# Optimization experiments

Hardware: AMD Instinct MI355X
Metric: run time of the kernel (lower is better)

The kernel has to match this reference:

```python
import jax, jax.numpy as jnp
import numpy as np

DIM = 128
HEADS = 4
WS = 7
SHIFT = 3
MLP_HIDDEN = 512
B, H, W = 8, 112, 112


def _rel_pos_index(ws):
    coords = np.stack(np.meshgrid(np.arange(ws), np.arange(ws), indexing='ij'))  # 2,ws,ws
    flat = coords.reshape(2, -1)  # 2, ws*ws
    rel = (flat[:, :, None] - flat[:, None, :]).transpose(1, 2, 0)  # N,N,2
    rel[:, :, 0] += ws - 1
    rel[:, :, 1] += ws - 1
    rel[:, :, 0] *= 2 * ws - 1
    return rel.sum(-1).astype(np.int32)  # N,N


def setup_inputs() -> dict:
    key = jax.random.key(0)
    ks = jax.random.split(key, 12)
    s = 0.02
    return {
        'x': jax.random.normal(ks[0], (B, DIM, H, W), jnp.float32),
        'norm1_g': jnp.ones((DIM,), jnp.float32),
        'norm1_b': jnp.zeros((DIM,), jnp.float32),
        'qkv_w': jax.random.normal(ks[1], (DIM, 3 * DIM), jnp.float32) * s,
        'qkv_b': jnp.zeros((3 * DIM,), jnp.float32),
        'rel_bias_table': jax.random.normal(ks[2], ((2 * WS - 1) ** 2, HEADS), jnp.float32) * s,
        'rel_index': jnp.asarray(_rel_pos_index(WS)),
        'proj_w': jax.random.normal(ks[3], (DIM, DIM), jnp.float32) * s,
        'proj_b': jnp.zeros((DIM,), jnp.float32),
        'norm2_g': jnp.ones((DIM,), jnp.float32),
        'norm2_b': jnp.zeros((DIM,), jnp.float32),
        'fc1_w': jax.random.normal(ks[4], (DIM, MLP_HIDDEN), jnp.float32) * s,
        'fc1_b': jnp.zeros((MLP_HIDDEN,), jnp.float32),
        'fc2_w': jax.random.normal(ks[5], (MLP_HIDDEN, DIM), jnp.float32) * s,
        'fc2_b': jnp.zeros((DIM,), jnp.float32),
    }


def _ln(x, g, b, eps=1e-5):
    m = jnp.mean(x, axis=-1, keepdims=True)
    v = jnp.var(x, axis=-1, keepdims=True)
    return (x - m) * jax.lax.rsqrt(v + eps) * g + b


def _swin_fwd(x, norm1_g, norm1_b, qkv_w, qkv_b, rel_bias_table, rel_index,
              proj_w, proj_b, norm2_g, norm2_b, fc1_w, fc1_b, fc2_w, fc2_b):
    Bb, C, Hh, Ww = x.shape
    x = x.reshape(Bb, C, Hh * Ww).transpose(0, 2, 1)  # B, L, C
    shortcut = x
    x = _ln(x, norm1_g, norm1_b)
    x = x.reshape(Bb, Hh, Ww, C)
    # H, W are multiples of WS here, so no padding needed (pad_r = pad_b = 0)
    if SHIFT > 0:
        x = jnp.roll(x, (-SHIFT, -SHIFT), axis=(1, 2))
    nH, nW = Hh // WS, Ww // WS
    # window partition -> (num_windows, N, C)
    xw = x.reshape(Bb, nH, WS, nW, WS, C).transpose(0, 1, 3, 2, 4, 5).reshape(-1, WS * WS, C)
    NWIN, N = xw.shape[0], WS * WS
    hd = C // HEADS
    qkv = (xw @ qkv_w + qkv_b).reshape(NWIN, N, 3, HEADS, hd).transpose(2, 0, 3, 1, 4)
    q, k, v = qkv[0], qkv[1], qkv[2]  # each (NWIN, HEADS, N, hd)
    scale = hd ** -0.5
    attn = jnp.einsum('whnd,whmd->whnm', q * scale, k)
    bias = rel_bias_table[rel_index.reshape(-1)].reshape(N, N, HEADS).transpose(2, 0, 1)
    attn = jax.nn.softmax(attn + bias[None], axis=-1)
    out = jnp.einsum('whnm,whmd->whnd', attn, v)  # NWIN, HEADS, N, hd
    out = out.transpose(0, 2, 1, 3).reshape(NWIN, N, C) @ proj_w + proj_b
    # window reverse
    x = out.reshape(Bb, nH, nW, WS, WS, C).transpose(0, 1, 3, 2, 4, 5).reshape(Bb, Hh, Ww, C)
    if SHIFT > 0:
        x = jnp.roll(x, (SHIFT, SHIFT), axis=(1, 2))
    x = x.reshape(Bb, Hh * Ww, C)
    x = shortcut + x
    h = _ln(x, norm2_g, norm2_b)
    h = jax.nn.gelu(h @ fc1_w + fc1_b, approximate=False) @ fc2_w + fc2_b
    x = x + h
    return x.transpose(0, 2, 1).reshape(Bb, C, Hh, Ww)


def reference(x, norm1_g, norm1_b, qkv_w, qkv_b, rel_bias_table, rel_index,
              proj_w, proj_b, norm2_g, norm2_b, fc1_w, fc1_b, fc2_w, fc2_b):
    return _swin_fwd(x, norm1_g, norm1_b, qkv_w, qkv_b, rel_bias_table, rel_index,
                     proj_w, proj_b, norm2_g, norm2_b, fc1_w, fc1_b, fc2_w, fc2_b)
```

## Files before the change

### kernel.cpp

```cpp
#include <hip/hip_runtime.h>
#include <hip/hip_bf16.h>
#include <math.h>

typedef __bf16 bf16;
typedef __bf16 bf16x8 __attribute__((ext_vector_type(8)));
typedef float f32x4 __attribute__((ext_vector_type(4)));

#define MFMA(a,b,c) __builtin_amdgcn_mfma_f32_16x16x32_bf16(a,b,c,0,0,0)

static __device__ __forceinline__ int swz256(int row, int kb){ return row*256 + (kb ^ ((row&7)<<4)); }
static __device__ __forceinline__ int swz128(int row, int kb){ return row*128 + (kb ^ ((row&7)<<4)); }
static __device__ __forceinline__ int swz64 (int row, int kb){ return row*64  + (kb ^ ((row&3)<<4)); }

__global__ void k_pack(const float* __restrict__ W, bf16* __restrict__ outp, int K, int N) {
    int idx = blockIdx.x*256 + threadIdx.x;
    int total = (N >> 4) * (K >> 5) * 64;
    if (idx >= total) return;
    int l = idx & 63, f = idx >> 6;
    int KF = K >> 5;
    int kf = f % KF, nf = f / KF;
    int n = nf*16 + (l & 15), k0 = kf*32 + (l >> 4)*8;
    bf16x8 v;
    for (int j = 0; j < 8; ++j) v[j] = (bf16)W[(size_t)(k0+j)*N + n];
    *(bf16x8*)(outp + (size_t)idx*8) = v;
}

__global__ void k_bias(const float* __restrict__ table, const int* __restrict__ ridx,
                       float* __restrict__ bias49) {
    int idx = blockIdx.x*256 + threadIdx.x;
    if (idx >= 2401) return;
    int ri = ridx[idx];
    for (int h = 0; h < 4; ++h) bias49[h*2401 + idx] = table[ri*4 + h];
}

__global__ void k_zero(uint4* __restrict__ xw4) {
    int idx = blockIdx.x*256 + threadIdx.x;
    if (idx >= 2048*240) return;
    int win = idx / 240, rem = idx - win*240;
    xw4[(size_t)win*1024 + 784 + rem] = make_uint4(0,0,0,0);
}

__global__ void __launch_bounds__(256) k_ln1(const float* __restrict__ x,
                                             const float* __restrict__ g1,
                                             const float* __restrict__ b1,
                                             bf16* __restrict__ xw) {
    __shared__ float T[128*113];
    __shared__ float meanL[112], rstdL[112];
    __shared__ float gL[128], bL[128];
    int tid = threadIdx.x;
    int b = blockIdx.x / 112, h = blockIdx.x - (blockIdx.x/112)*112;
    if (tid < 128) { gL[tid] = g1[tid]; bL[tid] = b1[tid]; }
    const float* xp = x + (size_t)b*128*12544 + h*112;
    for (int e = tid; e < 14336; e += 256) {
        int c = e / 112, w = e - c*112;
        T[c*113 + w] = xp[(size_t)c*12544 + w];
    }
    __syncthreads();
    if (tid < 224) {
        int w = tid >> 1, q = tid & 1;
        float s = 0.f, s2 = 0.f;
        for (int i = 0; i < 64; ++i) { float v = T[(q*64 + i)*113 + w]; s += v; s2 += v*v; }
        s  += __shfl_xor(s, 1, 64);
        s2 += __shfl_xor(s2, 1, 64);
        if (q == 0) {
            float m = s * 0.0078125f;
            float var = s2 * 0.0078125f - m*m;
            meanL[w] = m; rstdL[w] = rsqrtf(var + 1e-5f);
        }
    }
    __syncthreads();
    int hr = h + 109; if (hr >= 112) hr -= 112;
    int wh = hr / 7, nr = hr - wh*7;
    for (int e = tid; e < 14336; e += 256) {
        int w = e >> 7, c = e & 127;
        int wr = w + 109; if (wr >= 112) wr -= 112;
        int wwi = wr / 7, nc = wr - wwi*7;
        int win = b*256 + wh*16 + wwi;
        int n = nr*7 + nc;
        float v = (T[c*113 + w] - meanL[w]) * rstdL[w] * gL[c] + bL[c];
        xw[((size_t)win*64 + n)*128 + c] = (bf16)v;
    }
}

__global__ void __launch_bounds__(256, 4) k_attn(const bf16* __restrict__ xw,
                                              const bf16x8* __restrict__ wqkv,
                                              const float* __restrict__ qkv_b,
                                              const bf16x8* __restrict__ wproj,
                                              const float* __restrict__ proj_b,
                                              const float* __restrict__ bias49,
                                              bf16* __restrict__ x1p) {
    __shared__ char lds[49152];
    const int tid = threadIdx.x;
    const int l = tid & 63, wv = tid >> 6;
    const int win = blockIdx.x;
    const int lrow = l & 15, lk = l >> 4;
    char* X  = lds;
    char* VT = lds + wv*4096;
    char* Q  = lds + 16384 + wv*8192;
    char* Kt = Q + 4096;
    char* P  = Q;
    char* O  = lds + 16384;

    {
        const uint4* src = (const uint4*)(xw + (size_t)win*8192);
        for (int it = 0; it < 4; ++it) {
            int unit = it*256 + tid;
            int row = unit >> 4, s = unit & 15;
            *(uint4*)(X + swz256(row, s*16)) = src[unit];
        }
    }
    __syncthreads();

    {
        f32x4 qa[4][2], ka[4][2];
        float qb0 = qkv_b[      wv*32 + lrow], qb1 = qkv_b[      wv*32 + 16 + lrow];
        float kb0 = qkv_b[128 + wv*32 + lrow], kb1 = qkv_b[128 + wv*32 + 16 + lrow];
        for (int mf = 0; mf < 4; ++mf) for (int r = 0; r < 4; ++r) {
            qa[mf][0][r] = qb0; qa[mf][1][r] = qb1;
            ka[mf][0][r] = kb0; ka[mf][1][r] = kb1;
        }
        for (int kk = 0; kk < 4; ++kk) {
            bf16x8 a[4];
            for (int mf = 0; mf < 4; ++mf)
                a[mf] = *(const bf16x8*)(X + swz256(mf*16 + lrow, kk*64 + lk*16));
            for (int nf2 = 0; nf2 < 2; ++nf2) {
                bf16x8 bq = wqkv[(( (    wv*2 + nf2)*4 + kk)*64) + l];
                bf16x8 bk = wqkv[(( (8 + wv*2 + nf2)*4 + kk)*64) + l];
                for (int mf = 0; mf < 4; ++mf) {
                    qa[mf][nf2] = MFMA(a[mf], bq, qa[mf][nf2]);
                    ka[mf][nf2] = MFMA(a[mf], bk, ka[mf][nf2]);
                }
            }
        }
        const float scale = 0.17677669529663687f;
        for (int mf = 0; mf < 4; ++mf) for (int nf2 = 0; nf2 < 2; ++nf2)
            for (int r = 0; r < 4; ++r) {
                int row = mf*16 + lk*4 + r;
                int col = nf2*16 + lrow;
                *(bf16*)(Q  + swz64(row, col*2)) = (bf16)(qa[mf][nf2][r] * scale);
                *(bf16*)(Kt + swz64(row, col*2)) = (bf16)(ka[mf][nf2][r]);
            }
    }
    f32x4 va[4][2];
    {
        float vb0 = qkv_b[256 + wv*32 + lrow], vb1 = qkv_b[256 + wv*32 + 16 + lrow];
        for (int mf = 0; mf < 4; ++mf) for (int r = 0; r < 4; ++r) {
            va[mf][0][r] = vb0; va[mf][1][r] = vb1;
        }
        for (int kk = 0; kk < 4; ++kk) {
            bf16x8 a[4];
            for (int mf = 0; mf < 4; ++mf)
                a[mf] = *(const bf16x8*)(X + swz256(mf*16 + lrow, kk*64 + lk*16));
            for (int nf2 = 0; nf2 < 2; ++nf2) {
                bf16x8 bv = wqkv[(((16 + wv*2 + nf2)*4 + kk)*64) + l];
                for (int mf = 0; mf < 4; ++mf)
                    va[mf][nf2] = MFMA(a[mf], bv, va[mf][nf2]);
            }
        }
    }
    __syncthreads();
    for (int mf = 0; mf < 4; ++mf) for (int nf2 = 0; nf2 < 2; ++nf2)
        for (int r = 0; r < 4; ++r) {
            int row = mf*16 + lk*4 + r;
            int col = nf2*16 + lrow;
            *(bf16*)(VT + swz128(col, row*2)) = (bf16)(va[mf][nf2][r]);
        }

    f32x4 s[4][4];
    {
        const float* bh = bias49 + wv*2401;
        for (int mf = 0; mf < 4; ++mf) for (int nf = 0; nf < 4; ++nf)
            for (int r = 0; r < 4; ++r) {
                int row = mf*16 + lk*4 + r, col = nf*16 + lrow;
                float bv;
                if (col >= 49) bv = -1e30f;
                else if (row < 49) bv = bh[row*49 + col];
                else bv = 0.f;
                s[mf][nf][r] = bv;
            }
        bf16x8 aq[4], bk4[4];
        for (int mf = 0; mf < 4; ++mf) aq[mf]  = *(const bf16x8*)(Q  + swz64(mf*16 + lrow, lk*16));
        for (int nf = 0; nf < 4; ++nf) bk4[nf] = *(const bf16x8*)(Kt + swz64(nf*16 + lrow, lk*16));
        for (int mf = 0; mf < 4; ++mf) for (int nf = 0; nf < 4; ++nf)
            s[mf][nf] = MFMA(aq[mf], bk4[nf], s[mf][nf]);
    }
    for (int mf = 0; mf < 4; ++mf) for (int r = 0; r < 4; ++r) {
        float mx = -3e38f;
        for (int nf = 0; nf < 4; ++nf) mx = fmaxf(mx, s[mf][nf][r]);
        for (int d = 1; d < 16; d <<= 1) mx = fmaxf(mx, __shfl_xor(mx, d, 64));
        float sum = 0.f;
        for (int nf = 0; nf < 4; ++nf) { float p = __expf(s[mf][nf][r] - mx); s[mf][nf][r] = p; sum += p; }
        for (int d = 1; d < 16; d <<= 1) sum += __shfl_xor(sum, d, 64);
        float inv = 1.0f / sum;
        for (int nf = 0; nf < 4; ++nf) s[mf][nf][r] *= inv;
    }
    for (int mf = 0; mf < 4; ++mf) for (int nf = 0; nf < 4; ++nf)
        for (int r = 0; r < 4; ++r) {
            int row = mf*16 + lk*4 + r, col = nf*16 + lrow;
            *(bf16*)(P + swz128(row, col*2)) = (bf16)(s[mf][nf][r]);
        }

    f32x4 o[4][2];
    for (int mf = 0; mf < 4; ++mf) for (int nf = 0; nf < 2; ++nf)
        for (int r = 0; r < 4; ++r) o[mf][nf][r] = 0.f;
    for (int kf = 0; kf < 2; ++kf) {
        bf16x8 ap[4], bv2[2];
        for (int mf = 0; mf < 4; ++mf)
            ap[mf] = *(const bf16x8*)(P + swz128(mf*16 + lrow, kf*64 + lk*16));
        for (int nf = 0; nf < 2; ++nf)
            bv2[nf] = *(const bf16x8*)(VT + swz128(nf*16 + lrow, kf*64 + lk*16));
        for (int mf = 0; mf < 4; ++mf) for (int nf = 0; nf < 2; ++nf)
            o[mf][nf] = MFMA(ap[mf], bv2[nf], o[mf][nf]);
    }
    __syncthreads();
    for (int mf = 0; mf < 4; ++mf) for (int nf = 0; nf < 2; ++nf)
        for (int r = 0; r < 4; ++r) {
            int row = mf*16 + lk*4 + r, col = wv*32 + nf*16 + lrow;
            *(bf16*)(O + swz256(row, col*2)) = (bf16)(o[mf][nf][r]);
        }
    __syncthreads();

    f32x4 pr[4][2];
    {
        float pb0 = proj_b[wv*32 + lrow], pb1 = proj_b[wv*32 + 16 + lrow];
        for (int mf = 0; mf < 4; ++mf) for (int r = 0; r < 4; ++r) { pr[mf][0][r] = pb0; pr[mf][1][r] = pb1; }
    }
    for (int kk = 0; kk < 4; ++kk) {
        bf16x8 a[4];
        for (int mf = 0; mf < 4; ++mf)
            a[mf] = *(const bf16x8*)(O + swz256(mf*16 + lrow, kk*64 + lk*16));
        for (int nf = 0; nf < 2; ++nf) {
            bf16x8 bfr = wproj[(((wv*2 + nf)*4 + kk)*64) + l];
            for (int mf = 0; mf < 4; ++mf) pr[mf][nf] = MFMA(a[mf], bfr, pr[mf][nf]);
        }
    }
    {
        int b_ = win >> 8, wh = (win >> 4) & 15, ww = win & 15;
        for (int mf = 0; mf < 4; ++mf) for (int r = 0; r < 4; ++r) {
            int row = mf*16 + lk*4 + r;
            if (row < 49) {
                int nr = row / 7, nc = row - nr*7;
                int h = wh*7 + nr + 3; if (h >= 112) h -= 112;
                int w = ww*7 + nc + 3; if (w >= 112) w -= 112;
                size_t t = (size_t)b_*12544 + h*112 + w;
                for (int nf = 0; nf < 2; ++nf) {
                    int col = wv*32 + nf*16 + lrow;
                    x1p[t*128 + col] = (bf16)pr[mf][nf][r];
                }
            }
        }
    }
}

__global__ void __launch_bounds__(256, 4) k_mlp(const float* __restrict__ x,
                                             const bf16* __restrict__ x1p,
                                             const float* __restrict__ g2,
                                             const float* __restrict__ b2,
                                             const float* __restrict__ fc1_b,
                                             const float* __restrict__ fc2_b,
                                             const bf16x8* __restrict__ wfc1,
                                             const bf16x8* __restrict__ wfc2,
                                             float* __restrict__ out) {
    __shared__ char lds[49408];
    char* Xs = lds;
    char* XN = lds + 16384;
    char* Hq = lds + 32768;
    float* OT = (float*)(lds + 16384);

    int tid = threadIdx.x;
    int l = tid & 63, wv = tid >> 6;
    int lrow = l & 15, lk = l >> 4;
    int blk = blockIdx.x;
    int b = blk / 196;
    int l0 = (blk - b*196) * 64;
    const float* xb = x + (size_t)b*128*12544 + l0;
    const bf16* xpb = x1p + ((size_t)b*12544 + l0)*128;

    {
        int t = wv*16 + lrow;
        float s = 0.f, s2 = 0.f;
        #pragma unroll
        for (int kk = 0; kk < 4; ++kk) {
            int c0 = kk*32 + lk*8;
            bf16x8 xpv = *(const bf16x8*)(xpb + t*128 + c0);
            bf16x8 v8;
            #pragma unroll
            for (int j = 0; j < 8; ++j) {
                float v = xb[(size_t)(c0+j)*12544 + t] + (float)xpv[j];
                s += v; s2 += v*v;
                v8[j] = (bf16)v;
            }
            *(bf16x8*)(Xs + swz256(t, kk*64 + lk*16)) = v8;
        }
        s  += __shfl_xor(s, 16, 64);  s  += __shfl_xor(s, 32, 64);
        s2 += __shfl_xor(s2, 16, 64); s2 += __shfl_xor(s2, 32, 64);
        float m = s * 0.0078125f;
        float var = s2 * 0.0078125f - m*m;
        float rs = rsqrtf(var + 1e-5f);
        #pragma unroll
        for (int kk = 0; kk < 4; ++kk) {
            int c0 = kk*32 + lk*8;
            bf16x8 v8 = *(const bf16x8*)(Xs + swz256(t, kk*64 + lk*16));
            float4 gv0 = *(const float4*)(g2 + c0), gv1 = *(const float4*)(g2 + c0 + 4);
            float4 bv0 = *(const float4*)(b2 + c0), bv1 = *(const float4*)(b2 + c0 + 4);
            float gg[8] = {gv0.x,gv0.y,gv0.z,gv0.w,gv1.x,gv1.y,gv1.z,gv1.w};
            float bb[8] = {bv0.x,bv0.y,bv0.z,bv0.w,bv1.x,bv1.y,bv1.z,bv1.w};
            #pragma unroll
            for (int j = 0; j < 8; ++j)
                v8[j] = (bf16)(((float)v8[j] - m) * rs * gg[j] + bb[j]);
            *(bf16x8*)(XN + swz256(t, kk*64 + lk*16)) = v8;
        }
    }
    __syncthreads();

    f32x4 acc2[4][2];
    for (int mf = 0; mf < 4; ++mf) for (int nf = 0; nf < 2; ++nf) {
        float bv = fc2_b[wv*32 + nf*16 + lrow];
        for (int r = 0; r < 4; ++r) acc2[mf][nf][r] = bv;
    }
    for (int q = 0; q < 4; ++q) {
        f32x4 acc1[4][2];
        for (int mf = 0; mf < 4; ++mf) for (int nf = 0; nf < 2; ++nf) {
            float bv = fc1_b[q*128 + wv*32 + nf*16 + lrow];
            for (int r = 0; r < 4; ++r) acc1[mf][nf][r] = bv;
        }
        for (int kk = 0; kk < 4; ++kk) {
            bf16x8 a[4];
            for (int mf = 0; mf < 4; ++mf)
                a[mf] = *(const bf16x8*)(XN + swz256(mf*16 + lrow, kk*64 + lk*16));
            for (int nf = 0; nf < 2; ++nf) {
                int nfg = q*8 + wv*2 + nf;
                bf16x8 bw = wfc1[(nfg*4 + kk)*64 + l];
                for (int mf = 0; mf < 4; ++mf)
                    acc1[mf][nf] = MFMA(a[mf], bw, acc1[mf][nf]);
            }
        }
        if (q) __syncthreads();
        for (int mf = 0; mf < 4; ++mf) for (int nf = 0; nf < 2; ++nf)
            for (int r = 0; r < 4; ++r) {
                int row = mf*16 + lk*4 + r, col = wv*32 + nf*16 + lrow;
                float v = acc1[mf][nf][r];
                float u = 0.7978845608f * (v + 0.044715f * v*v*v);
                float e2 = __expf(2.f * u);
                float th = 1.f - 2.f / (e2 + 1.f);
                v = 0.5f * v * (1.f + th);
                *(bf16*)(Hq + swz256(row, col*2)) = (bf16)v;
            }
        __syncthreads();
        for (int kk = 0; kk < 4; ++kk) {
            bf16x8 a[4];
            for (int mf = 0; mf < 4; ++mf)
                a[mf] = *(const bf16x8*)(Hq + swz256(mf*16 + lrow, kk*64 + lk*16));
            for (int nf = 0; nf < 2; ++nf) {
                bf16x8 bw = wfc2[(((wv*2 + nf)*16 + q*4 + kk)*64) + l];
                for (int mf = 0; mf < 4; ++mf)
                    acc2[mf][nf] = MFMA(a[mf], bw, acc2[mf][nf]);
            }
        }
    }
    __syncthreads();

    for (int mf = 0; mf < 4; ++mf) for (int nf = 0; nf < 2; ++nf)
        for (int r = 0; r < 4; ++r) {
            int t = mf*16 + lk*4 + r, c = wv*32 + nf*16 + lrow;
            float v = acc2[mf][nf][r] + (float)*(const bf16*)(Xs + swz256(t, c*2));
            OT[t*129 + c] = v;
        }
    __syncthreads();
    for (int it = 0; it < 8; ++it) {
        int unit = it*256 + tid;
        int c = unit >> 4, i = unit & 15;
        float4 o;
        o.x = OT[(i*4+0)*129 + c];
        o.y = OT[(i*4+1)*129 + c];
        o.z = OT[(i*4+2)*129 + c];
        o.w = OT[(i*4+3)*129 + c];
        *(float4*)(out + (size_t)(b*128 + c)*12544 + l0 + i*4) = o;
    }
}

extern "C" void kernel_launch(void* const* d_in, const int* in_sizes, int n_in,
                              void* d_out, int out_size, void* d_ws, size_t ws_size,
                              hipStream_t stream) {
    const float* x      = (const float*)d_in[0];
    const float* n1g    = (const float*)d_in[1];
    const float* n1b    = (const float*)d_in[2];
    const float* qkv_w  = (const float*)d_in[3];
    const float* qkv_b  = (const float*)d_in[4];
    const float* rtab   = (const float*)d_in[5];
    const int*   ridx   = (const int*)  d_in[6];
    const float* proj_w = (const float*)d_in[7];
    const float* proj_b = (const float*)d_in[8];
    const float* n2g    = (const float*)d_in[9];
    const float* n2b    = (const float*)d_in[10];
    const float* fc1_w  = (const float*)d_in[11];
    const float* fc1_b  = (const float*)d_in[12];
    const float* fc2_w  = (const float*)d_in[13];
    const float* fc2_b  = (const float*)d_in[14];
    float* out = (float*)d_out;
    char* ws = (char*)d_ws;

    bf16*  xw     = (bf16*)(ws);
    bf16*  x1p    = (bf16*)(ws + 33554432);
    bf16*  wqkv   = (bf16*)(ws + 59244544);
    bf16*  wproj  = (bf16*)(ws + 59342848);
    bf16*  wfc1   = (bf16*)(ws + 59375616);
    bf16*  wfc2   = (bf16*)(ws + 59506688);
    float* bias49 = (float*)(ws + 59637760);

    hipLaunchKernelGGL(k_pack, dim3(24), dim3(256), 0, stream, qkv_w,  wqkv,  128, 384);
    hipLaunchKernelGGL(k_pack, dim3(8),  dim3(256), 0, stream, proj_w, wproj, 128, 128);
    hipLaunchKernelGGL(k_pack, dim3(32), dim3(256), 0, stream, fc1_w,  wfc1,  128, 512);
    hipLaunchKernelGGL(k_pack, dim3(32), dim3(256), 0, stream, fc2_w,  wfc2,  512, 128);
    hipLaunchKernelGGL(k_bias, dim3(10), dim3(256), 0, stream, rtab, ridx, bias49);
    hipLaunchKernelGGL(k_zero, dim3(1920), dim3(256), 0, stream, (uint4*)xw);
    hipLaunchKernelGGL(k_ln1,  dim3(896),  dim3(256), 0, stream, x, n1g, n1b, xw);
    hipLaunchKernelGGL(k_attn, dim3(2048), dim3(256), 0, stream, xw, (const bf16x8*)wqkv,
                       qkv_b, (const bf16x8*)wproj, proj_b, bias49, x1p);
    hipLaunchKernelGGL(k_mlp,  dim3(1568), dim3(256), 0, stream, x, x1p, n2g, n2b,
                       fc1_b, fc2_b, (const bf16x8*)wfc1, (const bf16x8*)wfc2, out);
}
```

Before: 293.5 us.

## Fold LayerNorm2 into fc1 weights and apply row stats after the GEMM

Folds the LN2 gain into the packed fc1 weights and precomputes per-output vectors (sum of g*W and b*W + fc1_b), so the MLP kernel feeds the raw residual sum straight into fc1 and applies mean and rstd as a rank-1 correction on the accumulators. This removes the normalized copy XN and its LDS pass, shrinking LDS use, which may raise occupancy. It also vectorizes the V-transpose LDS stores and the output transpose through a padded column-major staging tile. The trade-off is precision: the un-normalized bf16 input feeds the MFMA and the mean is subtracted after the GEMM, which can lose accuracy through cancellation.

After: 339.3 us. 1.16x slower.

```diff
diff --git a/kernel.cpp b/kernel.cpp
--- a/kernel.cpp
+++ b/kernel.cpp
@@ -3,6 +3,7 @@
 #include <math.h>
 
 typedef __bf16 bf16;
+typedef __bf16 bf16x4 __attribute__((ext_vector_type(4)));
 typedef __bf16 bf16x8 __attribute__((ext_vector_type(8)));
 typedef float f32x4 __attribute__((ext_vector_type(4)));
 
@@ -23,6 +24,31 @@
     bf16x8 v;
     for (int j = 0; j < 8; ++j) v[j] = (bf16)W[(size_t)(k0+j)*N + n];
     *(bf16x8*)(outp + (size_t)idx*8) = v;
+}
+
+__global__ void k_pack1(const float* __restrict__ W, const float* __restrict__ g2,
+                        bf16* __restrict__ outp) {
+    int idx = blockIdx.x*256 + threadIdx.x;
+    if (idx >= 32*4*64) return;
+    int l = idx & 63, f = idx >> 6;
+    int kf = f & 3, nf = f >> 2;
+    int n = nf*16 + (l & 15), k0 = kf*32 + (l >> 4)*8;
+    bf16x8 v;
+    for (int j = 0; j < 8; ++j) v[j] = (bf16)(W[(size_t)(k0+j)*512 + n] * g2[k0+j]);
+    *(bf16x8*)(outp + (size_t)idx*8) = v;
+}
+
+__global__ void k_fc1aux(const float* __restrict__ W1, const float* __restrict__ g2,
+                         const float* __restrict__ b2, const float* __restrict__ b1,
+                         float* __restrict__ uvec, float* __restrict__ wvec) {
+    int n = blockIdx.x*256 + threadIdx.x;
+    if (n >= 512) return;
+    float u = 0.f, w = 0.f;
+    for (int c = 0; c < 128; ++c) {
+        float wv = W1[(size_t)c*512 + n];
+        u += g2[c]*wv; w += b2[c]*wv;
+    }
+    uvec[n] = u; wvec[n] = w + b1[n];
 }
 
 __global__ void k_bias(const float* __restrict__ table, const int* __restrict__ ridx,
@@ -159,12 +185,13 @@
         }
     }
     __syncthreads();
-    for (int mf = 0; mf < 4; ++mf) for (int nf2 = 0; nf2 < 2; ++nf2)
-        for (int r = 0; r < 4; ++r) {
-            int row = mf*16 + lk*4 + r;
-            int col = nf2*16 + lrow;
-            *(bf16*)(VT + swz128(col, row*2)) = (bf16)(va[mf][nf2][r]);
-        }
+    for (int mf = 0; mf < 4; ++mf) for (int nf2 = 0; nf2 < 2; ++nf2) {
+        int row0 = mf*16 + lk*4;
+        int col = nf2*16 + lrow;
+        bf16x4 v4;
+        for (int r = 0; r < 4; ++r) v4[r] = (bf16)(va[mf][nf2][r]);
+        *(bf16x4*)(VT + swz128(col, row0*2)) = v4;
+    }
 
     f32x4 s[4][4];
     {
@@ -254,18 +281,18 @@
 
 __global__ void __launch_bounds__(256, 4) k_mlp(const float* __restrict__ x,
                                              const bf16* __restrict__ x1p,
-                                             const float* __restrict__ g2,
-                                             const float* __restrict__ b2,
-                                             const float* __restrict__ fc1_b,
+                                             const float* __restrict__ uvec,
+                                             const float* __restrict__ wvec,
                                              const float* __restrict__ fc2_b,
                                              const bf16x8* __restrict__ wfc1,
                                              const bf16x8* __restrict__ wfc2,
                                              float* __restrict__ out) {
-    __shared__ char lds[49408];
+    __shared__ char lds[34816];
     char* Xs = lds;
-    char* XN = lds + 16384;
-    char* Hq = lds + 32768;
-    float* OT = (float*)(lds + 16384);
+    char* Hq = lds + 16384;
+    float* statM = (float*)(lds + 32768);
+    float* statR = (float*)(lds + 33024);
+    float* OT = (float*)lds;
 
     int tid = threadIdx.x;
     int l = tid & 63, wv = tid >> 6;
@@ -294,21 +321,10 @@
         }
         s  += __shfl_xor(s, 16, 64);  s  += __shfl_xor(s, 32, 64);
         s2 += __shfl_xor(s2, 16, 64); s2 += __shfl_xor(s2, 32, 64);
-        float m = s * 0.0078125f;
-        float var = s2 * 0.0078125f - m*m;
-        float rs = rsqrtf(var + 1e-5f);
-        #pragma unroll
-        for (int kk = 0; kk < 4; ++kk) {
-            int c0 = kk*32 + lk*8;
-            bf16x8 v8 = *(const bf16x8*)(Xs + swz256(t, kk*64 + lk*16));
-            float4 gv0 = *(const float4*)(g2 + c0), gv1 = *(const float4*)(g2 + c0 + 4);
-            float4 bv0 = *(const float4*)(b2 + c0), bv1 = *(const float4*)(b2 + c0 + 4);
-            float gg[8] = {gv0.x,gv0.y,gv0.z,gv0.w,gv1.x,gv1.y,gv1.z,gv1.w};
-            float bb[8] = {bv0.x,bv0.y,bv0.z,bv0.w,bv1.x,bv1.y,bv1.z,bv1.w};
-            #pragma unroll
-            for (int j = 0; j < 8; ++j)
-                v8[j] = (bf16)(((float)v8[j] - m) * rs * gg[j] + bb[j]);
-            *(bf16x8*)(XN + swz256(t, kk*64 + lk*16)) = v8;
+        if (lk == 0) {
+            float m = s * 0.0078125f;
+            float var = s2 * 0.0078125f - m*m;
+            statM[t] = m; statR[t] = rsqrtf(var + 1e-5f);
         }
     }
     __syncthreads();
@@ -320,14 +336,12 @@
     }
     for (int q = 0; q < 4; ++q) {
         f32x4 acc1[4][2];
-        for (int mf = 0; mf < 4; ++mf) for (int nf = 0; nf < 2; ++nf) {
-            float bv = fc1_b[q*128 + wv*32 + nf*16 + lrow];
-            for (int r = 0; r < 4; ++r) acc1[mf][nf][r] = bv;
-        }
+        for (int mf = 0; mf < 4; ++mf) for (int nf = 0; nf < 2; ++nf)
+            for (int r = 0; r < 4; ++r) acc1[mf][nf][r] = 0.f;
         for (int kk = 0; kk < 4; ++kk) {
             bf16x8 a[4];
             for (int mf = 0; mf < 4; ++mf)
-                a[mf] = *(const bf16x8*)(XN + swz256(mf*16 + lrow, kk*64 + lk*16));
+                a[mf] = *(const bf16x8*)(Xs + swz256(mf*16 + lrow, kk*64 + lk*16));
             for (int nf = 0; nf < 2; ++nf) {
                 int nfg = q*8 + wv*2 + nf;
                 bf16x8 bw = wfc1[(nfg*4 + kk)*64 + l];
@@ -335,17 +349,26 @@
                     acc1[mf][nf] = MFMA(a[mf], bw, acc1[mf][nf]);
             }
         }
+        float uu[2], ww[2];
+        for (int nf = 0; nf < 2; ++nf) {
+            int n = q*128 + wv*32 + nf*16 + lrow;
+            uu[nf] = uvec[n]; ww[nf] = wvec[n];
+        }
         if (q) __syncthreads();
-        for (int mf = 0; mf < 4; ++mf) for (int nf = 0; nf < 2; ++nf)
-            for (int r = 0; r < 4; ++r) {
-                int row = mf*16 + lk*4 + r, col = wv*32 + nf*16 + lrow;
-                float v = acc1[mf][nf][r];
-                float u = 0.7978845608f * (v + 0.044715f * v*v*v);
-                float e2 = __expf(2.f * u);
-                float th = 1.f - 2.f / (e2 + 1.f);
-                v = 0.5f * v * (1.f + th);
-                *(bf16*)(Hq + swz256(row, col*2)) = (bf16)v;
-            }
+        for (int mf = 0; mf < 4; ++mf) {
+            f32x4 m4 = *(const f32x4*)(statM + mf*16 + lk*4);
+            f32x4 r4 = *(const f32x4*)(statR + mf*16 + lk*4);
+            for (int nf = 0; nf < 2; ++nf)
+                for (int r = 0; r < 4; ++r) {
+                    int row = mf*16 + lk*4 + r, col = wv*32 + nf*16 + lrow;
+                    float v = (acc1[mf][nf][r] - m4[r]*uu[nf]) * r4[r] + ww[nf];
+                    float u = 0.7978845608f * (v + 0.044715f * v*v*v);
+                    float e2 = __expf(2.f * u);
+                    float th = 1.f - 2.f / (e2 + 1.f);
+                    v = 0.5f * v * (1.f + th);
+                    *(bf16*)(Hq + swz256(row, col*2)) = (bf16)v;
+                }
+        }
         __syncthreads();
         for (int kk = 0; kk < 4; ++kk) {
             bf16x8 a[4];
@@ -358,24 +381,23 @@
             }
         }
     }
-    __syncthreads();
 
     for (int mf = 0; mf < 4; ++mf) for (int nf = 0; nf < 2; ++nf)
         for (int r = 0; r < 4; ++r) {
             int t = mf*16 + lk*4 + r, c = wv*32 + nf*16 + lrow;
-            float v = acc2[mf][nf][r] + (float)*(const bf16*)(Xs + swz256(t, c*2));
-            OT[t*129 + c] = v;
-        }
+            acc2[mf][nf][r] += (float)*(const bf16*)(Xs + swz256(t, c*2));
+        }
+    __syncthreads();
+    for (int mf = 0; mf < 4; ++mf) for (int nf = 0; nf < 2; ++nf) {
+        int t0 = mf*16 + lk*4, c = wv*32 + nf*16 + lrow;
+        *(f32x4*)(OT + c*68 + t0) = acc2[mf][nf];
+    }
     __syncthreads();
     for (int it = 0; it < 8; ++it) {
         int unit = it*256 + tid;
         int c = unit >> 4, i = unit & 15;
-        float4 o;
-        o.x = OT[(i*4+0)*129 + c];
-        o.y = OT[(i*4+1)*129 + c];
-        o.z = OT[(i*4+2)*129 + c];
-        o.w = OT[(i*4+3)*129 + c];
-        *(float4*)(out + (size_t)(b*128 + c)*12544 + l0 + i*4) = o;
+        f32x4 o = *(const f32x4*)(OT + c*68 + i*4);
+        *(f32x4*)(out + (size_t)(b*128 + c)*12544 + l0 + i*4) = o;
     }
 }
 
@@ -407,16 +429,19 @@
     bf16*  wfc1   = (bf16*)(ws + 59375616);
     bf16*  wfc2   = (bf16*)(ws + 59506688);
     float* bias49 = (float*)(ws + 59637760);
-
-    hipLaunchKernelGGL(k_pack, dim3(24), dim3(256), 0, stream, qkv_w,  wqkv,  128, 384);
-    hipLaunchKernelGGL(k_pack, dim3(8),  dim3(256), 0, stream, proj_w, wproj, 128, 128);
-    hipLaunchKernelGGL(k_pack, dim3(32), dim3(256), 0, stream, fc1_w,  wfc1,  128, 512);
-    hipLaunchKernelGGL(k_pack, dim3(32), dim3(256), 0, stream, fc2_w,  wfc2,  512, 128);
-    hipLaunchKernelGGL(k_bias, dim3(10), dim3(256), 0, stream, rtab, ridx, bias49);
-    hipLaunchKernelGGL(k_zero, dim3(1920), dim3(256), 0, stream, (uint4*)xw);
-    hipLaunchKernelGGL(k_ln1,  dim3(896),  dim3(256), 0, stream, x, n1g, n1b, xw);
-    hipLaunchKernelGGL(k_attn, dim3(2048), dim3(256), 0, stream, xw, (const bf16x8*)wqkv,
+    float* uvec   = (float*)(ws + 59676672);
+    float* wvec   = (float*)(ws + 59678720);
+
+    hipLaunchKernelGGL(k_pack,   dim3(24), dim3(256), 0, stream, qkv_w,  wqkv,  128, 384);
+    hipLaunchKernelGGL(k_pack,   dim3(8),  dim3(256), 0, stream, proj_w, wproj, 128, 128);
+    hipLaunchKernelGGL(k_pack1,  dim3(32), dim3(256), 0, stream, fc1_w,  n2g, wfc1);
+    hipLaunchKernelGGL(k_pack,   dim3(32), dim3(256), 0, stream, fc2_w,  wfc2,  512, 128);
+    hipLaunchKernelGGL(k_fc1aux, dim3(2),  dim3(256), 0, stream, fc1_w, n2g, n2b, fc1_b, uvec, wvec);
+    hipLaunchKernelGGL(k_bias,   dim3(10), dim3(256), 0, stream, rtab, ridx, bias49);
+    hipLaunchKernelGGL(k_zero,   dim3(1920), dim3(256), 0, stream, (uint4*)xw);
+    hipLaunchKernelGGL(k_ln1,    dim3(896),  dim3(256), 0, stream, x, n1g, n1b, xw);
+    hipLaunchKernelGGL(k_attn,   dim3(2048), dim3(256), 0, stream, xw, (const bf16x8*)wqkv,
                        qkv_b, (const bf16x8*)wproj, proj_b, bias49, x1p);
-    hipLaunchKernelGGL(k_mlp,  dim3(1568), dim3(256), 0, stream, x, x1p, n2g, n2b,
-                       fc1_b, fc2_b, (const bf16x8*)wfc1, (const bf16x8*)wfc2, out);
-}
+    hipLaunchKernelGGL(k_mlp,    dim3(1568), dim3(256), 0, stream, x, x1p, uvec, wvec,
+                       fc2_b, (const bf16x8*)wfc1, (const bf16x8*)wfc2, out);
+}
```
